# Kernel optimization log

Hardware: AMD Instinct MI355X
Metric: run time of the kernel (lower is better)

Reference implementation:

```python
import jax, jax.numpy as jnp
import numpy as np

NUM_CAPSULE = 32
DIM_VECTOR = 16
NUM_ROUTING = 3

def squash(v, axis=-1):
    s2 = jnp.sum(jnp.square(v), axis=axis, keepdims=True)
    scale = s2 / (1.0 + s2) / jnp.sqrt(s2)
    return scale * v

def setup_inputs() -> dict:
    key = jax.random.key(0)
    k1, k2 = jax.random.split(key)
    B, IN_CAPS, IN_DIM = 64, 2048, 8
    x = jax.random.normal(k1, (B, IN_CAPS, IN_DIM), dtype=jnp.float32)
    # glorot-uniform-ish weight: [in_caps, num_caps, in_dim, out_dim]
    limit = np.sqrt(6.0 / (IN_DIM + DIM_VECTOR)).astype(np.float32)
    W = jax.random.uniform(k2, (IN_CAPS, NUM_CAPSULE, IN_DIM, DIM_VECTOR), dtype=jnp.float32, minval=-limit, maxval=limit)
    return {"x": x, "W": W}

def reference(x, W):
    # x: [B, in_caps, in_dim]; W: [in_caps, num_caps, in_dim, out_dim]
    # inputs_hat (u_hat): [B, in_caps, num_caps, out_dim]
    u_hat = jnp.einsum('bid,inde->bine', x, W)
    B, IN_CAPS = u_hat.shape[0], u_hat.shape[1]
    # routing logits; original broadcasts over out_dim with identical values,
    # so a trailing singleton dim is mathematically equivalent
    b = jnp.zeros((B, IN_CAPS, NUM_CAPSULE, 1), dtype=u_hat.dtype)
    v = None
    for i in range(NUM_ROUTING):
        c = jax.nn.softmax(b, axis=2)                       # over num_capsule
        s = jnp.sum(c * u_hat, axis=1, keepdims=True)       # [B,1,nc,out]
        v = squash(s)                                       # [B,1,nc,out]
        if i != NUM_ROUTING - 1:
            b = b + jnp.sum(u_hat * v, axis=-1, keepdims=True)
    return v.reshape(-1, NUM_CAPSULE, DIM_VECTOR)
```

## Files before the change

### kernel.cpp

```cpp
#include <hip/hip_runtime.h>
#include <math.h>


#define B_TOT 64
#define I_TOT 2048
#define D_IN  8
#define NC    32
#define EV    16
#define OD    (NC*EV)
#define BC    8
#define NBC   (B_TOT/BC)
#define BC0   16
#define NBC0  (B_TOT/BC0)
#define ICH   8
#define NIC   (I_TOT/ICH)
#define S_ELEMS (B_TOT*OD)

__device__ __forceinline__ void fma4(float4& acc, float a, const float4& w) {
    acc.x = fmaf(a, w.x, acc.x);
    acc.y = fmaf(a, w.y, acc.y);
    acc.z = fmaf(a, w.z, acc.z);
    acc.w = fmaf(a, w.w, acc.w);
}

__global__ void zero_s(float* __restrict__ s)
{
    s[(size_t)blockIdx.x * 256 + threadIdx.x] = 0.f;
}

__global__ __launch_bounds__(256, 4)
void route0(const float* __restrict__ x, const float* __restrict__ W,
            float* __restrict__ P)
{
    __shared__ __align__(16) float xl[BC0 * ICH * D_IN];

    const int t  = threadIdx.x;
    const int ic = blockIdx.x & (NIC - 1);
    const int bc = blockIdx.x >> 8;
    const int b0 = bc * BC0;
    const int i0 = ic * ICH;
    const int eq = t & 3;
    const int bh = (t >> 2) & 1;
    const int n  = t >> 3;

    {
        const int row = t >> 4, f = (t & 15) * 4;
        *(float4*)&xl[row * (ICH * D_IN) + f] =
            *(const float4*)&x[((size_t)(b0 + row) * I_TOT + i0) * D_IN + f];
    }
    __syncthreads();

    float4 sacc[8];
    #pragma unroll
    for (int q = 0; q < 8; ++q) sacc[q] = make_float4(0.f, 0.f, 0.f, 0.f);

    const float* Wt = &W[(size_t)i0 * 4096 + n * 128 + eq * 4];

    #pragma unroll 1
    for (int ii = 0; ii < ICH; ++ii) {
        float4 wr[8];
        #pragma unroll
        for (int d = 0; d < 8; ++d)
            wr[d] = *(const float4*)&Wt[ii * 4096 + d * 16];

        #pragma unroll
        for (int q = 0; q < 8; ++q) {
            const int bl = bh * 8 + q;
            float4 xa = *(float4*)&xl[bl * (ICH * D_IN) + ii * 8];
            float4 xb = *(float4*)&xl[bl * (ICH * D_IN) + ii * 8 + 4];
            fma4(sacc[q], xa.x, wr[0]); fma4(sacc[q], xa.y, wr[1]);
            fma4(sacc[q], xa.z, wr[2]); fma4(sacc[q], xa.w, wr[3]);
            fma4(sacc[q], xb.x, wr[4]); fma4(sacc[q], xb.y, wr[5]);
            fma4(sacc[q], xb.z, wr[6]); fma4(sacc[q], xb.w, wr[7]);
        }
    }

    #pragma unroll
    for (int q = 0; q < 8; ++q)
        *(float4*)&P[((size_t)ic * B_TOT + b0 + bh * 8 + q) * OD + n * EV + eq * 4] = sacc[q];
}

__global__ __launch_bounds__(256, 4)
void route1(const float* __restrict__ x, const float* __restrict__ W,
            float* __restrict__ P, const float* __restrict__ vin)
{
    __shared__ __align__(16) float xl[BC * ICH * D_IN];
    __shared__ float wsum[2][4][BC];

    const int t  = threadIdx.x;
    const int ic = blockIdx.x & (NIC - 1);
    const int bc = blockIdx.x >> 8;
    const int b0 = bc * BC;
    const int i0 = ic * ICH;
    const int eq = t & 3;
    const int bh = (t >> 2) & 1;
    const int n  = t >> 3;
    const int w  = t >> 6;

    if (t < 128) {
        const int row = t >> 4, f = (t & 15) * 4;
        *(float4*)&xl[row * (ICH * D_IN) + f] =
            *(const float4*)&x[((size_t)(b0 + row) * I_TOT + i0) * D_IN + f];
    }

    float4 vr[4];
    #pragma unroll
    for (int q = 0; q < 4; ++q)
        vr[q] = *(const float4*)&vin[(size_t)(b0 + bh * 4 + q) * OD + n * EV + eq * 4];
    __syncthreads();

    float4 sacc[4];
    #pragma unroll
    for (int q = 0; q < 4; ++q) sacc[q] = make_float4(0.f, 0.f, 0.f, 0.f);

    const float* Wt = &W[(size_t)i0 * 4096 + n * 128 + eq * 4];

    #pragma unroll 1
    for (int ii = 0; ii < ICH; ++ii) {
        float4 wr[8];
        #pragma unroll
        for (int d = 0; d < 8; ++d)
            wr[d] = *(const float4*)&Wt[ii * 4096 + d * 16];

        float4 u[4];
        #pragma unroll
        for (int q = 0; q < 4; ++q) {
            const int bl = bh * 4 + q;
            float4 xa = *(float4*)&xl[bl * (ICH * D_IN) + ii * 8];
            float4 xb = *(float4*)&xl[bl * (ICH * D_IN) + ii * 8 + 4];
            float4 uu = make_float4(0.f, 0.f, 0.f, 0.f);
            fma4(uu, xa.x, wr[0]); fma4(uu, xa.y, wr[1]);
            fma4(uu, xa.z, wr[2]); fma4(uu, xa.w, wr[3]);
            fma4(uu, xb.x, wr[4]); fma4(uu, xb.y, wr[5]);
            fma4(uu, xb.z, wr[6]); fma4(uu, xb.w, wr[7]);
            u[q] = uu;
        }

        float a[4];
        #pragma unroll
        for (int q = 0; q < 4; ++q) {
            float ap = u[q].x * vr[q].x + u[q].y * vr[q].y
                     + u[q].z * vr[q].z + u[q].w * vr[q].w;
            ap += __shfl_xor(ap, 1, 64);
            ap += __shfl_xor(ap, 2, 64);
            a[q] = ap;
        }
        float e[4], p[4];
        #pragma unroll
        for (int q = 0; q < 4; ++q) {
            e[q] = __expf(a[q]);
            float pp = e[q];
            pp += __shfl_xor(pp, 8, 64);
            pp += __shfl_xor(pp, 16, 64);
            pp += __shfl_xor(pp, 32, 64);
            p[q] = pp;
        }
        if (eq == 0) {
            #pragma unroll
            for (int q = 0; q < 4; ++q)
                wsum[ii & 1][w][bh * 4 + q] = p[q];
        }
        __syncthreads();
        #pragma unroll
        for (int q = 0; q < 4; ++q) {
            const int bl = bh * 4 + q;
            float s = wsum[ii & 1][0][bl] + wsum[ii & 1][1][bl]
                    + wsum[ii & 1][2][bl] + wsum[ii & 1][3][bl];
            float c = e[q] / s;
            fma4(sacc[q], c, u[q]);
        }
    }

    #pragma unroll
    for (int q = 0; q < 4; ++q)
        *(float4*)&P[((size_t)ic * B_TOT + b0 + bh * 4 + q) * OD + n * EV + eq * 4] = sacc[q];
}

__global__ __launch_bounds__(256, 4)
void reduce_p(const float* __restrict__ P, float* __restrict__ s)
{
    __shared__ float red[256];
    const int b   = blockIdx.x >> 5;
    const int oq  = (blockIdx.x >> 2) & 7;
    const int icq = blockIdx.x & 3;
    const int t   = threadIdx.x;
    const int o   = oq * 64 + (t & 63);
    const int sub = t >> 6;
    const size_t stride = (size_t)B_TOT * OD;

    float acc = 0.f;
    size_t base = ((size_t)(icq * 64 + sub * 16) * B_TOT + b) * OD + o;
    #pragma unroll
    for (int k = 0; k < 16; ++k) acc += P[base + (size_t)k * stride];
    red[t] = acc;
    __syncthreads();
    if (t < 64) {
        float v = red[t] + red[t + 64] + red[t + 128] + red[t + 192];
        atomicAdd(&s[(size_t)b * OD + o], v);
    }
}

__global__ __launch_bounds__(64, 8)
void squash_k(const float* __restrict__ s, float* __restrict__ dst,
              const float* __restrict__ addsrc, float pre)
{
    const int b = blockIdx.x >> 3;
    const int o = (blockIdx.x & 7) * 64 + threadIdx.x;
    float v = s[(size_t)b * OD + o] * pre;
    float q2 = v * v;
    q2 += __shfl_xor(q2, 1, 64);
    q2 += __shfl_xor(q2, 2, 64);
    q2 += __shfl_xor(q2, 4, 64);
    q2 += __shfl_xor(q2, 8, 64);
    float sc = q2 / ((1.0f + q2) * sqrtf(q2));
    float outv = v * sc;
    if (addsrc) outv += addsrc[(size_t)b * OD + o];
    dst[(size_t)b * OD + o] = outv;
}

extern "C" void kernel_launch(void* const* d_in, const int* in_sizes, int n_in,
                              void* d_out, int out_size, void* d_ws, size_t ws_size,
                              hipStream_t stream) {
    const float* x = (const float*)d_in[0];
    const float* W = (const float*)d_in[1];
    float* out = (float*)d_out;

    char* ws = (char*)d_ws;
    float* P  = (float*)ws;
    float* s0 = (float*)(ws + (size_t)32 * 1024 * 1024);
    float* s1 = s0 + S_ELEMS;
    float* s2 = s1 + S_ELEMS;
    float* v0 = s2 + S_ELEMS;
    float* vs = v0 + S_ELEMS;

    dim3 r0g(NBC0 * NIC), r1g(NBC * NIC), rb(256);
    dim3 dg(B_TOT * 8 * 4), db(256);
    dim3 sg(B_TOT * 8), sb(64);

    zero_s<<<dim3(3 * S_ELEMS / 256), dim3(256), 0, stream>>>(s0);

    route0<<<r0g, rb, 0, stream>>>(x, W, P);
    reduce_p<<<dg, db, 0, stream>>>(P, s0);
    squash_k<<<sg, sb, 0, stream>>>(s0, v0, nullptr, 1.0f / 32.0f);
    route1<<<r1g, rb, 0, stream>>>(x, W, P, v0);
    reduce_p<<<dg, db, 0, stream>>>(P, s1);
    squash_k<<<sg, sb, 0, stream>>>(s1, vs, v0, 1.0f);
    route1<<<r1g, rb, 0, stream>>>(x, W, P, vs);
    reduce_p<<<dg, db, 0, stream>>>(P, s2);
    squash_k<<<sg, sb, 0, stream>>>(s2, out, nullptr, 1.0f);
}
```

Measured before the change: 190.2 us.

## Fuse squash into routing and reduction kernels, drop atomics and zeroing

Folds the squash step into the start of each routing kernel and into the final reduction, which removes the separate squash launches and the intermediate v buffers. The reduction now sums all 256 partial chunks in a single block per output tile and writes directly, so the zeroing kernel and the atomicAdds go away. The softmax division also switches to a fast approximate divide. In exchange, every route1 block recomputes the squash redundantly, and the reduction has fewer, longer-running blocks.

```diff
diff --git a/kernel.cpp b/kernel.cpp
--- a/kernel.cpp
+++ b/kernel.cpp
@@ -23,11 +23,6 @@
     acc.w = fmaf(a, w.w, acc.w);
 }
 
-__global__ void zero_s(float* __restrict__ s)
-{
-    s[(size_t)blockIdx.x * 256 + threadIdx.x] = 0.f;
-}
-
 __global__ __launch_bounds__(256, 4)
 void route0(const float* __restrict__ x, const float* __restrict__ W,
             float* __restrict__ P)
@@ -80,9 +75,11 @@
         *(float4*)&P[((size_t)ic * B_TOT + b0 + bh * 8 + q) * OD + n * EV + eq * 4] = sacc[q];
 }
 
+template <int NS>
 __global__ __launch_bounds__(256, 4)
 void route1(const float* __restrict__ x, const float* __restrict__ W,
-            float* __restrict__ P, const float* __restrict__ vin)
+            float* __restrict__ P, const float* __restrict__ s0,
+            const float* __restrict__ s1, float pre0)
 {
     __shared__ __align__(16) float xl[BC * ICH * D_IN];
     __shared__ float wsum[2][4][BC];
@@ -105,8 +102,26 @@
 
     float4 vr[4];
     #pragma unroll
-    for (int q = 0; q < 4; ++q)
-        vr[q] = *(const float4*)&vin[(size_t)(b0 + bh * 4 + q) * OD + n * EV + eq * 4];
+    for (int q = 0; q < 4; ++q) {
+        const size_t off = (size_t)(b0 + bh * 4 + q) * OD + n * EV + eq * 4;
+        float4 t0 = *(const float4*)&s0[off];
+        t0.x *= pre0; t0.y *= pre0; t0.z *= pre0; t0.w *= pre0;
+        float q2 = t0.x*t0.x + t0.y*t0.y + t0.z*t0.z + t0.w*t0.w;
+        q2 += __shfl_xor(q2, 1, 64);
+        q2 += __shfl_xor(q2, 2, 64);
+        float sc = q2 / ((1.0f + q2) * sqrtf(q2));
+        float4 v = make_float4(t0.x*sc, t0.y*sc, t0.z*sc, t0.w*sc);
+        if (NS == 2) {
+            float4 t1 = *(const float4*)&s1[off];
+            float r2 = t1.x*t1.x + t1.y*t1.y + t1.z*t1.z + t1.w*t1.w;
+            r2 += __shfl_xor(r2, 1, 64);
+            r2 += __shfl_xor(r2, 2, 64);
+            float sc1 = r2 / ((1.0f + r2) * sqrtf(r2));
+            v.x = fmaf(t1.x, sc1, v.x); v.y = fmaf(t1.y, sc1, v.y);
+            v.z = fmaf(t1.z, sc1, v.z); v.w = fmaf(t1.w, sc1, v.w);
+        }
+        vr[q] = v;
+    }
     __syncthreads();
 
     float4 sacc[4];
@@ -166,7 +181,7 @@
             const int bl = bh * 4 + q;
             float s = wsum[ii & 1][0][bl] + wsum[ii & 1][1][bl]
                     + wsum[ii & 1][2][bl] + wsum[ii & 1][3][bl];
-            float c = e[q] / s;
+            float c = __fdividef(e[q], s);
             fma4(sacc[q], c, u[q]);
         }
     }
@@ -177,45 +192,54 @@
 }
 
 __global__ __launch_bounds__(256, 4)
-void reduce_p(const float* __restrict__ P, float* __restrict__ s)
+void reduce_s(const float* __restrict__ P, float* __restrict__ s)
 {
     __shared__ float red[256];
-    const int b   = blockIdx.x >> 5;
-    const int oq  = (blockIdx.x >> 2) & 7;
-    const int icq = blockIdx.x & 3;
+    const int b   = blockIdx.x >> 3;
+    const int oq  = blockIdx.x & 7;
     const int t   = threadIdx.x;
     const int o   = oq * 64 + (t & 63);
-    const int sub = t >> 6;
+    const int icq = t >> 6;
     const size_t stride = (size_t)B_TOT * OD;
 
     float acc = 0.f;
-    size_t base = ((size_t)(icq * 64 + sub * 16) * B_TOT + b) * OD + o;
-    #pragma unroll
-    for (int k = 0; k < 16; ++k) acc += P[base + (size_t)k * stride];
+    size_t base = ((size_t)(icq * 64) * B_TOT + b) * OD + o;
+    #pragma unroll 8
+    for (int k = 0; k < 64; ++k) acc += P[base + (size_t)k * stride];
     red[t] = acc;
     __syncthreads();
+    if (t < 64)
+        s[(size_t)b * OD + o] = red[t] + red[t + 64] + red[t + 128] + red[t + 192];
+}
+
+__global__ __launch_bounds__(256, 4)
+void reduce_squash(const float* __restrict__ P, float* __restrict__ dst)
+{
+    __shared__ float red[256];
+    const int b   = blockIdx.x >> 3;
+    const int oq  = blockIdx.x & 7;
+    const int t   = threadIdx.x;
+    const int o   = oq * 64 + (t & 63);
+    const int icq = t >> 6;
+    const size_t stride = (size_t)B_TOT * OD;
+
+    float acc = 0.f;
+    size_t base = ((size_t)(icq * 64) * B_TOT + b) * OD + o;
+    #pragma unroll 8
+    for (int k = 0; k < 64; ++k) acc += P[base + (size_t)k * stride];
+    red[t] = acc;
+    __syncthreads();
+
     if (t < 64) {
         float v = red[t] + red[t + 64] + red[t + 128] + red[t + 192];
-        atomicAdd(&s[(size_t)b * OD + o], v);
-    }
-}
-
-__global__ __launch_bounds__(64, 8)
-void squash_k(const float* __restrict__ s, float* __restrict__ dst,
-              const float* __restrict__ addsrc, float pre)
-{
-    const int b = blockIdx.x >> 3;
-    const int o = (blockIdx.x & 7) * 64 + threadIdx.x;
-    float v = s[(size_t)b * OD + o] * pre;
-    float q2 = v * v;
-    q2 += __shfl_xor(q2, 1, 64);
-    q2 += __shfl_xor(q2, 2, 64);
-    q2 += __shfl_xor(q2, 4, 64);
-    q2 += __shfl_xor(q2, 8, 64);
-    float sc = q2 / ((1.0f + q2) * sqrtf(q2));
-    float outv = v * sc;
-    if (addsrc) outv += addsrc[(size_t)b * OD + o];
-    dst[(size_t)b * OD + o] = outv;
+        float q2 = v * v;
+        q2 += __shfl_xor(q2, 1, 64);
+        q2 += __shfl_xor(q2, 2, 64);
+        q2 += __shfl_xor(q2, 4, 64);
+        q2 += __shfl_xor(q2, 8, 64);
+        float sc = q2 / ((1.0f + q2) * sqrtf(q2));
+        dst[(size_t)b * OD + o] = v * sc;
+    }
 }
 
 extern "C" void kernel_launch(void* const* d_in, const int* in_sizes, int n_in,
@@ -229,23 +253,14 @@
     float* P  = (float*)ws;
     float* s0 = (float*)(ws + (size_t)32 * 1024 * 1024);
     float* s1 = s0 + S_ELEMS;
-    float* s2 = s1 + S_ELEMS;
-    float* v0 = s2 + S_ELEMS;
-    float* vs = v0 + S_ELEMS;
 
     dim3 r0g(NBC0 * NIC), r1g(NBC * NIC), rb(256);
-    dim3 dg(B_TOT * 8 * 4), db(256);
-    dim3 sg(B_TOT * 8), sb(64);
-
-    zero_s<<<dim3(3 * S_ELEMS / 256), dim3(256), 0, stream>>>(s0);
+    dim3 sg(B_TOT * 8), sb(256);
 
     route0<<<r0g, rb, 0, stream>>>(x, W, P);
-    reduce_p<<<dg, db, 0, stream>>>(P, s0);
-    squash_k<<<sg, sb, 0, stream>>>(s0, v0, nullptr, 1.0f / 32.0f);
-    route1<<<r1g, rb, 0, stream>>>(x, W, P, v0);
-    reduce_p<<<dg, db, 0, stream>>>(P, s1);
-    squash_k<<<sg, sb, 0, stream>>>(s1, vs, v0, 1.0f);
-    route1<<<r1g, rb, 0, stream>>>(x, W, P, vs);
-    reduce_p<<<dg, db, 0, stream>>>(P, s2);
-    squash_k<<<sg, sb, 0, stream>>>(s2, out, nullptr, 1.0f);
-}
+    reduce_s<<<sg, sb, 0, stream>>>(P, s0);
+    route1<1><<<r1g, rb, 0, stream>>>(x, W, P, s0, nullptr, 1.0f / 32.0f);
+    reduce_s<<<sg, sb, 0, stream>>>(P, s1);
+    route1<2><<<r1g, rb, 0, stream>>>(x, W, P, s0, s1, 1.0f / 32.0f);
+    reduce_squash<<<sg, sb, 0, stream>>>(P, out);
+}
```

Result: no change. 191.9 us (+0.9%).

## Fuse reduction with squash, drop zeroing and atomics, widen route1 batch tile

Applied to the files above, without the earlier changes.

The cross-chunk reduction and the squash step now run in one kernel that sums all 256 partial chunks per output without atomics. This removes the zeroing kernel and three squash launches. route1 now handles 16 batches per block in two halves, so each W load is reused across twice as many batches, and it uses a fast divide. Both route kernels also stagger the per-block order of the inner-capsule loop to spread W accesses. The cost is fewer reduce blocks, each with a longer serial loop, and two barriers per iteration in route1.

```diff
diff --git a/kernel.cpp b/kernel.cpp
--- a/kernel.cpp
+++ b/kernel.cpp
@@ -8,10 +8,8 @@
 #define NC    32
 #define EV    16
 #define OD    (NC*EV)
-#define BC    8
+#define BC    16
 #define NBC   (B_TOT/BC)
-#define BC0   16
-#define NBC0  (B_TOT/BC0)
 #define ICH   8
 #define NIC   (I_TOT/ICH)
 #define S_ELEMS (B_TOT*OD)
@@ -23,21 +21,16 @@
     acc.w = fmaf(a, w.w, acc.w);
 }
 
-__global__ void zero_s(float* __restrict__ s)
-{
-    s[(size_t)blockIdx.x * 256 + threadIdx.x] = 0.f;
-}
-
 __global__ __launch_bounds__(256, 4)
 void route0(const float* __restrict__ x, const float* __restrict__ W,
             float* __restrict__ P)
 {
-    __shared__ __align__(16) float xl[BC0 * ICH * D_IN];
+    __shared__ __align__(16) float xl[BC * ICH * D_IN];
 
     const int t  = threadIdx.x;
     const int ic = blockIdx.x & (NIC - 1);
     const int bc = blockIdx.x >> 8;
-    const int b0 = bc * BC0;
+    const int b0 = bc * BC;
     const int i0 = ic * ICH;
     const int eq = t & 3;
     const int bh = (t >> 2) & 1;
@@ -58,16 +51,17 @@
 
     #pragma unroll 1
     for (int ii = 0; ii < ICH; ++ii) {
+        const int iir = (ii + bc * 2) & 7;
         float4 wr[8];
         #pragma unroll
         for (int d = 0; d < 8; ++d)
-            wr[d] = *(const float4*)&Wt[ii * 4096 + d * 16];
+            wr[d] = *(const float4*)&Wt[iir * 4096 + d * 16];
 
         #pragma unroll
         for (int q = 0; q < 8; ++q) {
             const int bl = bh * 8 + q;
-            float4 xa = *(float4*)&xl[bl * (ICH * D_IN) + ii * 8];
-            float4 xb = *(float4*)&xl[bl * (ICH * D_IN) + ii * 8 + 4];
+            float4 xa = *(float4*)&xl[bl * (ICH * D_IN) + iir * 8];
+            float4 xb = *(float4*)&xl[bl * (ICH * D_IN) + iir * 8 + 4];
             fma4(sacc[q], xa.x, wr[0]); fma4(sacc[q], xa.y, wr[1]);
             fma4(sacc[q], xa.z, wr[2]); fma4(sacc[q], xa.w, wr[3]);
             fma4(sacc[q], xb.x, wr[4]); fma4(sacc[q], xb.y, wr[5]);
@@ -85,7 +79,7 @@
             float* __restrict__ P, const float* __restrict__ vin)
 {
     __shared__ __align__(16) float xl[BC * ICH * D_IN];
-    __shared__ float wsum[2][4][BC];
+    __shared__ float wsum[2][4][8];
 
     const int t  = threadIdx.x;
     const int ic = blockIdx.x & (NIC - 1);
@@ -97,125 +91,124 @@
     const int n  = t >> 3;
     const int w  = t >> 6;
 
-    if (t < 128) {
+    {
         const int row = t >> 4, f = (t & 15) * 4;
         *(float4*)&xl[row * (ICH * D_IN) + f] =
             *(const float4*)&x[((size_t)(b0 + row) * I_TOT + i0) * D_IN + f];
     }
-
-    float4 vr[4];
-    #pragma unroll
-    for (int q = 0; q < 4; ++q)
-        vr[q] = *(const float4*)&vin[(size_t)(b0 + bh * 4 + q) * OD + n * EV + eq * 4];
     __syncthreads();
 
-    float4 sacc[4];
-    #pragma unroll
-    for (int q = 0; q < 4; ++q) sacc[q] = make_float4(0.f, 0.f, 0.f, 0.f);
+    float4 sacc[8];
+    #pragma unroll
+    for (int q = 0; q < 8; ++q) sacc[q] = make_float4(0.f, 0.f, 0.f, 0.f);
 
     const float* Wt = &W[(size_t)i0 * 4096 + n * 128 + eq * 4];
+    const float* vb = &vin[(size_t)b0 * OD + n * EV + eq * 4];
 
     #pragma unroll 1
     for (int ii = 0; ii < ICH; ++ii) {
+        const int iir = (ii + bc * 2) & 7;
         float4 wr[8];
         #pragma unroll
         for (int d = 0; d < 8; ++d)
-            wr[d] = *(const float4*)&Wt[ii * 4096 + d * 16];
-
-        float4 u[4];
-        #pragma unroll
-        for (int q = 0; q < 4; ++q) {
-            const int bl = bh * 4 + q;
-            float4 xa = *(float4*)&xl[bl * (ICH * D_IN) + ii * 8];
-            float4 xb = *(float4*)&xl[bl * (ICH * D_IN) + ii * 8 + 4];
-            float4 uu = make_float4(0.f, 0.f, 0.f, 0.f);
-            fma4(uu, xa.x, wr[0]); fma4(uu, xa.y, wr[1]);
-            fma4(uu, xa.z, wr[2]); fma4(uu, xa.w, wr[3]);
-            fma4(uu, xb.x, wr[4]); fma4(uu, xb.y, wr[5]);
-            fma4(uu, xb.z, wr[6]); fma4(uu, xb.w, wr[7]);
-            u[q] = uu;
+            wr[d] = *(const float4*)&Wt[iir * 4096 + d * 16];
+
+        #pragma unroll
+        for (int h = 0; h < 2; ++h) {
+            float4 vv[4];
+            #pragma unroll
+            for (int q = 0; q < 4; ++q)
+                vv[q] = *(const float4*)&vb[(size_t)(h * 8 + bh * 4 + q) * OD];
+
+            float4 u[4];
+            #pragma unroll
+            for (int q = 0; q < 4; ++q) {
+                const int bl = h * 8 + bh * 4 + q;
+                float4 xa = *(float4*)&xl[bl * (ICH * D_IN) + iir * 8];
+                float4 xb = *(float4*)&xl[bl * (ICH * D_IN) + iir * 8 + 4];
+                float4 uu = make_float4(0.f, 0.f, 0.f, 0.f);
+                fma4(uu, xa.x, wr[0]); fma4(uu, xa.y, wr[1]);
+                fma4(uu, xa.z, wr[2]); fma4(uu, xa.w, wr[3]);
+                fma4(uu, xb.x, wr[4]); fma4(uu, xb.y, wr[5]);
+                fma4(uu, xb.z, wr[6]); fma4(uu, xb.w, wr[7]);
+                u[q] = uu;
+            }
+
+            float a[4];
+            #pragma unroll
+            for (int q = 0; q < 4; ++q) {
+                float ap = u[q].x * vv[q].x + u[q].y * vv[q].y
+                         + u[q].z * vv[q].z + u[q].w * vv[q].w;
+                ap += __shfl_xor(ap, 1, 64);
+                ap += __shfl_xor(ap, 2, 64);
+                a[q] = ap;
+            }
+            float e[4], p[4];
+            #pragma unroll
+            for (int q = 0; q < 4; ++q) {
+                e[q] = __expf(a[q]);
+                float pp = e[q];
+                pp += __shfl_xor(pp, 8, 64);
+                pp += __shfl_xor(pp, 16, 64);
+                pp += __shfl_xor(pp, 32, 64);
+                p[q] = pp;
+            }
+            if (eq == 0) {
+                #pragma unroll
+                for (int q = 0; q < 4; ++q)
+                    wsum[h][w][bh * 4 + q] = p[q];
+            }
+            __syncthreads();
+            #pragma unroll
+            for (int q = 0; q < 4; ++q) {
+                const int rl = bh * 4 + q;
+                float s = wsum[h][0][rl] + wsum[h][1][rl]
+                        + wsum[h][2][rl] + wsum[h][3][rl];
+                float c = __fdividef(e[q], s);
+                fma4(sacc[h * 4 + q], c, u[q]);
+            }
         }
-
-        float a[4];
-        #pragma unroll
-        for (int q = 0; q < 4; ++q) {
-            float ap = u[q].x * vr[q].x + u[q].y * vr[q].y
-                     + u[q].z * vr[q].z + u[q].w * vr[q].w;
-            ap += __shfl_xor(ap, 1, 64);
-            ap += __shfl_xor(ap, 2, 64);
-            a[q] = ap;
-        }
-        float e[4], p[4];
-        #pragma unroll
-        for (int q = 0; q < 4; ++q) {
-            e[q] = __expf(a[q]);
-            float pp = e[q];
-            pp += __shfl_xor(pp, 8, 64);
-            pp += __shfl_xor(pp, 16, 64);
-            pp += __shfl_xor(pp, 32, 64);
-            p[q] = pp;
-        }
-        if (eq == 0) {
-            #pragma unroll
-            for (int q = 0; q < 4; ++q)
-                wsum[ii & 1][w][bh * 4 + q] = p[q];
-        }
-        __syncthreads();
-        #pragma unroll
-        for (int q = 0; q < 4; ++q) {
-            const int bl = bh * 4 + q;
-            float s = wsum[ii & 1][0][bl] + wsum[ii & 1][1][bl]
-                    + wsum[ii & 1][2][bl] + wsum[ii & 1][3][bl];
-            float c = e[q] / s;
-            fma4(sacc[q], c, u[q]);
-        }
-    }
-
-    #pragma unroll
-    for (int q = 0; q < 4; ++q)
-        *(float4*)&P[((size_t)ic * B_TOT + b0 + bh * 4 + q) * OD + n * EV + eq * 4] = sacc[q];
+    }
+
+    #pragma unroll
+    for (int h = 0; h < 2; ++h)
+        #pragma unroll
+        for (int q = 0; q < 4; ++q)
+            *(float4*)&P[((size_t)ic * B_TOT + b0 + h * 8 + bh * 4 + q) * OD
+                         + n * EV + eq * 4] = sacc[h * 4 + q];
 }
 
 __global__ __launch_bounds__(256, 4)
-void reduce_p(const float* __restrict__ P, float* __restrict__ s)
+void reduce_sq(const float* __restrict__ P, float* __restrict__ dst,
+               const float* __restrict__ addsrc, float pre)
 {
     __shared__ float red[256];
-    const int b   = blockIdx.x >> 5;
-    const int oq  = (blockIdx.x >> 2) & 7;
-    const int icq = blockIdx.x & 3;
+    const int b   = blockIdx.x >> 3;
+    const int oq  = blockIdx.x & 7;
     const int t   = threadIdx.x;
     const int o   = oq * 64 + (t & 63);
-    const int sub = t >> 6;
+    const int icq = t >> 6;
     const size_t stride = (size_t)B_TOT * OD;
 
     float acc = 0.f;
-    size_t base = ((size_t)(icq * 64 + sub * 16) * B_TOT + b) * OD + o;
-    #pragma unroll
-    for (int k = 0; k < 16; ++k) acc += P[base + (size_t)k * stride];
+    size_t base = ((size_t)(icq * 64) * B_TOT + b) * OD + o;
+    #pragma unroll 8
+    for (int k = 0; k < 64; ++k) acc += P[base + (size_t)k * stride];
     red[t] = acc;
     __syncthreads();
+
     if (t < 64) {
-        float v = red[t] + red[t + 64] + red[t + 128] + red[t + 192];
-        atomicAdd(&s[(size_t)b * OD + o], v);
-    }
-}
-
-__global__ __launch_bounds__(64, 8)
-void squash_k(const float* __restrict__ s, float* __restrict__ dst,
-              const float* __restrict__ addsrc, float pre)
-{
-    const int b = blockIdx.x >> 3;
-    const int o = (blockIdx.x & 7) * 64 + threadIdx.x;
-    float v = s[(size_t)b * OD + o] * pre;
-    float q2 = v * v;
-    q2 += __shfl_xor(q2, 1, 64);
-    q2 += __shfl_xor(q2, 2, 64);
-    q2 += __shfl_xor(q2, 4, 64);
-    q2 += __shfl_xor(q2, 8, 64);
-    float sc = q2 / ((1.0f + q2) * sqrtf(q2));
-    float outv = v * sc;
-    if (addsrc) outv += addsrc[(size_t)b * OD + o];
-    dst[(size_t)b * OD + o] = outv;
+        float v = (red[t] + red[t + 64] + red[t + 128] + red[t + 192]) * pre;
+        float q2 = v * v;
+        q2 += __shfl_xor(q2, 1, 64);
+        q2 += __shfl_xor(q2, 2, 64);
+        q2 += __shfl_xor(q2, 4, 64);
+        q2 += __shfl_xor(q2, 8, 64);
+        float sc = q2 / ((1.0f + q2) * sqrtf(q2));
+        float outv = v * sc;
+        if (addsrc) outv += addsrc[(size_t)b * OD + o];
+        dst[(size_t)b * OD + o] = outv;
+    }
 }
 
 extern "C" void kernel_launch(void* const* d_in, const int* in_sizes, int n_in,
@@ -227,25 +220,16 @@
 
     char* ws = (char*)d_ws;
     float* P  = (float*)ws;
-    float* s0 = (float*)(ws + (size_t)32 * 1024 * 1024);
-    float* s1 = s0 + S_ELEMS;
-    float* s2 = s1 + S_ELEMS;
-    float* v0 = s2 + S_ELEMS;
+    float* v0 = (float*)(ws + (size_t)32 * 1024 * 1024);
     float* vs = v0 + S_ELEMS;
 
-    dim3 r0g(NBC0 * NIC), r1g(NBC * NIC), rb(256);
-    dim3 dg(B_TOT * 8 * 4), db(256);
-    dim3 sg(B_TOT * 8), sb(64);
-
-    zero_s<<<dim3(3 * S_ELEMS / 256), dim3(256), 0, stream>>>(s0);
-
-    route0<<<r0g, rb, 0, stream>>>(x, W, P);
-    reduce_p<<<dg, db, 0, stream>>>(P, s0);
-    squash_k<<<sg, sb, 0, stream>>>(s0, v0, nullptr, 1.0f / 32.0f);
-    route1<<<r1g, rb, 0, stream>>>(x, W, P, v0);
-    reduce_p<<<dg, db, 0, stream>>>(P, s1);
-    squash_k<<<sg, sb, 0, stream>>>(s1, vs, v0, 1.0f);
-    route1<<<r1g, rb, 0, stream>>>(x, W, P, vs);
-    reduce_p<<<dg, db, 0, stream>>>(P, s2);
-    squash_k<<<sg, sb, 0, stream>>>(s2, out, nullptr, 1.0f);
-}
+    dim3 rg(NBC * NIC), rb(256);
+    dim3 sg(B_TOT * 8), sb(256);
+
+    route0<<<rg, rb, 0, stream>>>(x, W, P);
+    reduce_sq<<<sg, sb, 0, stream>>>(P, v0, nullptr, 1.0f / 32.0f);
+    route1<<<rg, rb, 0, stream>>>(x, W, P, v0);
+    reduce_sq<<<sg, sb, 0, stream>>>(P, vs, v0, 1.0f);
+    route1<<<rg, rb, 0, stream>>>(x, W, P, vs);
+    reduce_sq<<<sg, sb, 0, stream>>>(P, out, nullptr, 1.0f);
+}
```

New measurement: 257.9 us. 1.36x slower.
